# Performance work log

Measured on AMD Instinct MI355X. Metric: run time of the kernel, lower is better.

## Reference

```python
import jax, jax.numpy as jnp
import numpy as np

LAYERS, BLOCKS = 10, 4
RC, DC, SC, EC = 32, 32, 256, 256  # residual, dilation, skip, end channels
CIN, COUT, K = 6, 1, 2
DILATIONS = [2 ** (i % LAYERS) for i in range(BLOCKS * LAYERS)]
NL = len(DILATIONS)


def conv1d(x, w, dilation=1, pad=0):
    # x: [N, C, T], w: [O, I, K]
    return jax.lax.conv_general_dilated(
        x, w, window_strides=(1,), padding=[(pad, pad)],
        rhs_dilation=(dilation,), dimension_numbers=('NCH', 'OIH', 'NCH'))


def setup_inputs() -> dict:
    key = jax.random.key(0)
    ks = jax.random.split(key, 10)
    s = 0.1
    return {
        'x': jax.random.normal(ks[0], (8, CIN, 8192), dtype=jnp.float32),
        'start_w': jax.random.normal(ks[1], (RC, CIN, 1), dtype=jnp.float32) * s,
        'filter_w': jax.random.normal(ks[2], (NL, DC, RC, K), dtype=jnp.float32) * s,
        'gate_w': jax.random.normal(ks[3], (NL, DC, RC, K), dtype=jnp.float32) * s,
        'res_w': jax.random.normal(ks[4], (NL, RC, DC, 1), dtype=jnp.float32) * s,
        'skip_w': jax.random.normal(ks[5], (NL, SC, DC, 1), dtype=jnp.float32) * s,
        'end1_w': jax.random.normal(ks[6], (EC, SC, 1), dtype=jnp.float32) * s,
        'end1_b': jax.random.normal(ks[7], (EC,), dtype=jnp.float32) * s,
        'end2_w': jax.random.normal(ks[8], (COUT, EC, 1), dtype=jnp.float32) * s,
        'end2_b': jax.random.normal(ks[9], (COUT,), dtype=jnp.float32) * s,
    }


def reference(x, start_w, filter_w, gate_w, res_w, skip_w, end1_w, end1_b, end2_w, end2_b):
    x = conv1d(x, start_w)  # [B, RC, T]
    T = x.shape[2]
    # symmetric padding=(K-1)*d makes length grow by d each layer;
    # the shortest skip is the first one: T + (K-1)*DILATIONS[0]
    min_len = T + (K - 1) * DILATIONS[0]
    skip_sum = jnp.zeros((x.shape[0], SC, min_len), dtype=x.dtype)
    for i, d in enumerate(DILATIONS):
        pad = (K - 1) * d
        f = jnp.tanh(conv1d(x, filter_w[i], d, pad))
        g = jax.nn.sigmoid(conv1d(x, gate_w[i], d, pad))
        x = f * g  # [B, DC, T'] with T' = T_prev + d
        s = conv1d(x, skip_w[i])
        skip_sum = skip_sum + s[:, :, -min_len:]
        x = conv1d(x, res_w[i]) + x  # residual add (RC == DC)
    h = jax.nn.relu(skip_sum)
    h = jax.nn.relu(conv1d(h, end1_w) + end1_b[None, :, None])
    h = conv1d(h, end2_w) + end2_b[None, :, None]
    return h[:, :, -1]  # [B, COUT]
```

## Files before the change

kernel.cpp:

```cpp
#include <hip/hip_runtime.h>
#include <hip/hip_fp16.h>
#include <math.h>


#define NL 40
#define TLEN 8192

#define F_BLOB 0
#define F_C0   61440
#define F_Z    61696
#define F_H    71936
#define F_OB   73984
#define F_CNT  73992

__device__ __forceinline__ float wsrc(const float* __restrict__ fw,
                                      const float* __restrict__ gw,
                                      const float* __restrict__ rw,
                                      int l, int ch, int h, int r) {
    const int base = (l * 32 + ch) * 32 + h * 16;
    if (r < 16) return fw[(base + r) * 2];
    if (r < 32) return gw[(base + (r - 16)) * 2];
    return rw[base + (r - 32)];
}

__global__ __launch_bounds__(256) void k1_prep(
    const float* __restrict__ x, const float* __restrict__ start_w,
    const float* __restrict__ filter_w, const float* __restrict__ gate_w,
    const float* __restrict__ res_w, float* __restrict__ ws)
{
    const int blk = blockIdx.x, t = threadIdx.x;
    if (blk < 240) {
        const int p = blk * 256 + t;
        const int l = p / 1536;
        const int rem = p - l * 1536;
        const int i = rem >> 8;
        const int rem2 = rem & 255;
        const int lane = rem2 >> 2;
        const int jp = rem2 & 3;
        const int ch = lane & 31, h = lane >> 5;
        const int r0 = i * 8 + jp * 2;
        const float v0 = wsrc(filter_w, gate_w, res_w, l, ch, h, r0);
        const float v1 = wsrc(filter_w, gate_w, res_w, l, ch, h, r0 + 1);
        ((__half2*)ws)[p] = __floats2half2_rn(v0, v1);
    } else {
        const int b = t >> 5, ch = t & 31;
        float acc = 0.f;
#pragma unroll
        for (int j = 0; j < 6; ++j)
            acc += start_w[ch * 6 + j] * x[(b * 6 + j) * TLEN + TLEN - 1];
        ws[F_C0 + t] = acc;
#pragma unroll
        for (int k = t; k < 2048; k += 256) ws[F_H + k] = 0.f;
        if (t < 8) { ws[F_OB + t] = 0.f; ((int*)(ws + F_CNT))[t] = 0; }
    }
}

struct WBlob { float4 q[6]; };

__device__ __forceinline__ float dot16h(const float4& a, const float4& b,
                                        const float* c) {
    const __half2* h0 = (const __half2*)&a;
    const __half2* h1 = (const __half2*)&b;
    float acc = 0.f;
#pragma unroll
    for (int i = 0; i < 4; ++i) {
        float2 w = __half22float2(h0[i]);
        acc += w.x * c[2*i] + w.y * c[2*i+1];
    }
#pragma unroll
    for (int i = 0; i < 4; ++i) {
        float2 w = __half22float2(h1[i]);
        acc += w.x * c[8+2*i] + w.y * c[8+2*i+1];
    }
    return acc;
}

__device__ __forceinline__ float tanh_fast(float f) {
    f = fminf(fmaxf(f, -15.f), 15.f);
    float e2 = __expf(2.f * f);
    return (e2 - 1.f) / (e2 + 1.f);
}

#define K2_PREFETCH(L4, D) do {                                              \
    if ((L4) < NL) {                                                         \
        _Pragma("unroll")                                                    \
        for (int i = 0; i < 6; ++i)                                          \
            w##D.q[i] = blob[(L4) * 384 + i * 64 + lane];                    \
    }                                                                        \
} while (0)

#define K2_STEP(L, D) do {                                                   \
    float cc[16];                                                            \
    { const float4* cp = (const float4*)(cs + h * 16);                       \
      _Pragma("unroll")                                                      \
      for (int i = 0; i < 4; ++i) ((float4*)cc)[i] = cp[i]; }                \
    float f = dot16h(w##D.q[0], w##D.q[1], cc);                              \
    float g = dot16h(w##D.q[2], w##D.q[3], cc);                              \
    f += __shfl_xor(f, 32, 64);                                              \
    g += __shfl_xor(g, 32, 64);                                              \
    float z = tanh_fast(f) * (1.f / (1.f + __expf(-g)));                     \
    if (h == 0) { zs[ch] = z; zbuf[((L) * 8 + b) * 32 + ch] = z; }           \
    __builtin_amdgcn_wave_barrier();                                         \
    float zz[16];                                                            \
    { const float4* zp = (const float4*)(zs + h * 16);                       \
      _Pragma("unroll")                                                      \
      for (int i = 0; i < 4; ++i) ((float4*)zz)[i] = zp[i]; }                \
    float r = dot16h(w##D.q[4], w##D.q[5], zz);                              \
    r += __shfl_xor(r, 32, 64);                                              \
    float cnew = r + z;                                                      \
    __builtin_amdgcn_wave_barrier();                                         \
    if (h == 0) cs[ch] = cnew;                                               \
    __builtin_amdgcn_wave_barrier();                                         \
    K2_PREFETCH((L) + 4, D);                                                 \
} while (0)

__global__ __launch_bounds__(512) void k2_recur(float* __restrict__ ws)
{
    const int t = threadIdx.x;
    const int b = t >> 6;
    const int lane = t & 63;
    const int ch = lane & 31, h = lane >> 5;

    __shared__ float csm[8][32];
    __shared__ float zsm[8][32];
    float* cs = csm[b];
    float* zs = zsm[b];
    float* zbuf = ws + F_Z;

    if (h == 0) cs[ch] = ws[F_C0 + b * 32 + ch];
    __builtin_amdgcn_wave_barrier();

    const float4* blob = (const float4*)ws;
    WBlob w0, w1, w2, w3;
    K2_PREFETCH(0, 0);
    K2_PREFETCH(1, 1);
    K2_PREFETCH(2, 2);
    K2_PREFETCH(3, 3);

    for (int l = 0; l < NL; l += 4) {
        K2_STEP(l + 0, 0);
        K2_STEP(l + 1, 1);
        K2_STEP(l + 2, 2);
        K2_STEP(l + 3, 3);
    }
}

__global__ __launch_bounds__(256) void k3a_skip(
    const float* __restrict__ skip_w, float* __restrict__ ws)
{
    const int l = blockIdx.x, b = blockIdx.y, t = threadIdx.x;
    __shared__ __align__(16) float zsm[32];
    if (t < 32) zsm[t] = ws[F_Z + (l * 8 + b) * 32 + t];
    __syncthreads();
    const float4* w4 = (const float4*)(skip_w + (size_t)(l * 256 + t) * 32);
    const float4* z4 = (const float4*)zsm;
    float acc = 0.f;
#pragma unroll
    for (int i = 0; i < 8; ++i) {
        float4 wv = w4[i], zv = z4[i];
        acc += wv.x*zv.x + wv.y*zv.y + wv.z*zv.z + wv.w*zv.w;
    }
    atomicAdd(&ws[F_H + b * 256 + t], acc);
}

__global__ __launch_bounds__(256) void k3b_end(
    const float* __restrict__ end1_w, const float* __restrict__ end1_b,
    const float* __restrict__ end2_w, const float* __restrict__ end2_b,
    float* __restrict__ ws, float* __restrict__ out)
{
    const int q = blockIdx.x, b = blockIdx.y, t = threadIdx.x;
    __shared__ __align__(16) float hsm[256];
    __shared__ float psum[64][5];
    const int p = t >> 6, oc = t & 63, row = q * 64 + oc;

    float4 wreg[16];
    const float4* wp = (const float4*)(end1_w + (size_t)row * 256 + p * 64);
#pragma unroll
    for (int i = 0; i < 16; ++i) wreg[i] = wp[i];

    hsm[t] = fmaxf(ws[F_H + b * 256 + t], 0.f);
    __syncthreads();
    const float4* h4 = (const float4*)(hsm + p * 64);
    float acc = 0.f;
#pragma unroll
    for (int i = 0; i < 16; ++i) {
        float4 wv = wreg[i], hv = h4[i];
        acc += wv.x*hv.x + wv.y*hv.y + wv.z*hv.z + wv.w*hv.w;
    }
    psum[oc][p] = acc;
    __syncthreads();
    if (t < 64) {
        const int rr = q * 64 + t;
        float e = psum[t][0] + psum[t][1] + psum[t][2] + psum[t][3]
                + end1_b[rr];
        e = fmaxf(e, 0.f);
        float pe = e * end2_w[rr];
#pragma unroll
        for (int off = 32; off > 0; off >>= 1)
            pe += __shfl_down(pe, off, 64);
        if (t == 0) {
            float* obuf = ws + F_OB;
            int* cnt = (int*)(ws + F_CNT);
            atomicAdd(&obuf[b], pe);
            __threadfence();
            int old = __hip_atomic_fetch_add(&cnt[b], 1, __ATOMIC_ACQ_REL,
                                             __HIP_MEMORY_SCOPE_AGENT);
            if (old == 3) {
                float tot = __hip_atomic_load(&obuf[b], __ATOMIC_ACQUIRE,
                                              __HIP_MEMORY_SCOPE_AGENT);
                out[b] = tot + end2_b[0];
            }
        }
    }
}

extern "C" void kernel_launch(void* const* d_in, const int* in_sizes, int n_in,
                              void* d_out, int out_size, void* d_ws, size_t ws_size,
                              hipStream_t stream) {
    const float* x        = (const float*)d_in[0];
    const float* start_w  = (const float*)d_in[1];
    const float* filter_w = (const float*)d_in[2];
    const float* gate_w   = (const float*)d_in[3];
    const float* res_w    = (const float*)d_in[4];
    const float* skip_w   = (const float*)d_in[5];
    const float* end1_w   = (const float*)d_in[6];
    const float* end1_b   = (const float*)d_in[7];
    const float* end2_w   = (const float*)d_in[8];
    const float* end2_b   = (const float*)d_in[9];
    float* out = (float*)d_out;
    float* ws  = (float*)d_ws;

    k1_prep <<<241, 256, 0, stream>>>(x, start_w, filter_w, gate_w, res_w, ws);
    k2_recur<<<1, 512, 0, stream>>>(ws);
    k3a_skip<<<dim3(NL, 8), 256, 0, stream>>>(skip_w, ws);
    k3b_end <<<dim3(4, 8), 256, 0, stream>>>(end1_w, end1_b, end2_w, end2_b,
                                             ws, out);
}
```

Before: 107.5 us.

## Merge four kernels into two using spin-wait magic flags between blocks

New measurement: 117.6 us. +9.4%, slower.

```diff
diff --git a/kernel.cpp b/kernel.cpp
--- a/kernel.cpp
+++ b/kernel.cpp
@@ -5,13 +5,27 @@
 
 #define NL 40
 #define TLEN 8192
+#define MAGIC 0x13572468
+#define POLL_SLEEP 4
 
 #define F_BLOB 0
-#define F_C0   61440
-#define F_Z    61696
-#define F_H    71936
-#define F_OB   73984
-#define F_CNT  73992
+#define F_Z    61440
+#define F_H    71680
+#define F_OB   73728
+#define F_FLAG 73736
+
+__device__ __forceinline__ void wait_magic(const int* p) {
+    while (__hip_atomic_load(p, __ATOMIC_RELAXED, __HIP_MEMORY_SCOPE_AGENT)
+           != MAGIC)
+        __builtin_amdgcn_s_sleep(POLL_SLEEP);
+    (void)__hip_atomic_load(p, __ATOMIC_ACQUIRE, __HIP_MEMORY_SCOPE_AGENT);
+}
+__device__ __forceinline__ void set_magic(int* p) {
+    __hip_atomic_store(p, MAGIC, __ATOMIC_RELEASE, __HIP_MEMORY_SCOPE_AGENT);
+}
+__device__ __forceinline__ float ldf(const float* p) {
+    return __hip_atomic_load(p, __ATOMIC_RELAXED, __HIP_MEMORY_SCOPE_AGENT);
+}
 
 __device__ __forceinline__ float wsrc(const float* __restrict__ fw,
                                       const float* __restrict__ gw,
@@ -21,38 +35,6 @@
     if (r < 16) return fw[(base + r) * 2];
     if (r < 32) return gw[(base + (r - 16)) * 2];
     return rw[base + (r - 32)];
-}
-
-__global__ __launch_bounds__(256) void k1_prep(
-    const float* __restrict__ x, const float* __restrict__ start_w,
-    const float* __restrict__ filter_w, const float* __restrict__ gate_w,
-    const float* __restrict__ res_w, float* __restrict__ ws)
-{
-    const int blk = blockIdx.x, t = threadIdx.x;
-    if (blk < 240) {
-        const int p = blk * 256 + t;
-        const int l = p / 1536;
-        const int rem = p - l * 1536;
-        const int i = rem >> 8;
-        const int rem2 = rem & 255;
-        const int lane = rem2 >> 2;
-        const int jp = rem2 & 3;
-        const int ch = lane & 31, h = lane >> 5;
-        const int r0 = i * 8 + jp * 2;
-        const float v0 = wsrc(filter_w, gate_w, res_w, l, ch, h, r0);
-        const float v1 = wsrc(filter_w, gate_w, res_w, l, ch, h, r0 + 1);
-        ((__half2*)ws)[p] = __floats2half2_rn(v0, v1);
-    } else {
-        const int b = t >> 5, ch = t & 31;
-        float acc = 0.f;
-#pragma unroll
-        for (int j = 0; j < 6; ++j)
-            acc += start_w[ch * 6 + j] * x[(b * 6 + j) * TLEN + TLEN - 1];
-        ws[F_C0 + t] = acc;
-#pragma unroll
-        for (int k = t; k < 2048; k += 256) ws[F_H + k] = 0.f;
-        if (t < 8) { ws[F_OB + t] = 0.f; ((int*)(ws + F_CNT))[t] = 0; }
-    }
 }
 
 struct WBlob { float4 q[6]; };
@@ -114,9 +96,32 @@
     K2_PREFETCH((L) + 4, D);                                                 \
 } while (0)
 
-__global__ __launch_bounds__(512) void k2_recur(float* __restrict__ ws)
+__global__ __launch_bounds__(512) void ka_repack_recur(
+    const float* __restrict__ x, const float* __restrict__ start_w,
+    const float* __restrict__ filter_w, const float* __restrict__ gate_w,
+    const float* __restrict__ res_w, float* __restrict__ ws)
 {
-    const int t = threadIdx.x;
+    const int blk = blockIdx.x, t = threadIdx.x;
+    int* wf = (int*)(ws + F_FLAG);
+
+    if (blk < 120) {
+        const int p = blk * 512 + t;
+        const int l = p / 1536;
+        const int rem = p - l * 1536;
+        const int i = rem >> 8;
+        const int rem2 = rem & 255;
+        const int lane = rem2 >> 2;
+        const int jp = rem2 & 3;
+        const int ch = lane & 31, h = lane >> 5;
+        const int r0 = i * 8 + jp * 2;
+        const float v0 = wsrc(filter_w, gate_w, res_w, l, ch, h, r0);
+        const float v1 = wsrc(filter_w, gate_w, res_w, l, ch, h, r0 + 1);
+        ((__half2*)ws)[p] = __floats2half2_rn(v0, v1);
+        __syncthreads();
+        if (t == 0) set_magic(&wf[blk]);
+        return;
+    }
+
     const int b = t >> 6;
     const int lane = t & 63;
     const int ch = lane & 31, h = lane >> 5;
@@ -127,8 +132,19 @@
     float* zs = zsm[b];
     float* zbuf = ws + F_Z;
 
-    if (h == 0) cs[ch] = ws[F_C0 + b * 32 + ch];
-    __builtin_amdgcn_wave_barrier();
+    for (int k = t; k < 2048; k += 512) ws[F_H + k] = 0.f;
+    if (t < 8) ws[F_OB + t] = 0.f;
+
+    if (h == 0) {
+        float acc = 0.f;
+#pragma unroll
+        for (int j = 0; j < 6; ++j)
+            acc += start_w[ch * 6 + j] * x[(b * 6 + j) * TLEN + TLEN - 1];
+        cs[ch] = acc;
+    }
+
+    if (t < 120) wait_magic(&wf[t]);
+    __syncthreads();
 
     const float4* blob = (const float4*)ws;
     WBlob w0, w1, w2, w3;
@@ -136,7 +152,6 @@
     K2_PREFETCH(1, 1);
     K2_PREFETCH(2, 2);
     K2_PREFETCH(3, 3);
-
     for (int l = 0; l < NL; l += 4) {
         K2_STEP(l + 0, 0);
         K2_STEP(l + 1, 1);
@@ -145,41 +160,52 @@
     }
 }
 
-__global__ __launch_bounds__(256) void k3a_skip(
-    const float* __restrict__ skip_w, float* __restrict__ ws)
-{
-    const int l = blockIdx.x, b = blockIdx.y, t = threadIdx.x;
-    __shared__ __align__(16) float zsm[32];
-    if (t < 32) zsm[t] = ws[F_Z + (l * 8 + b) * 32 + t];
-    __syncthreads();
-    const float4* w4 = (const float4*)(skip_w + (size_t)(l * 256 + t) * 32);
-    const float4* z4 = (const float4*)zsm;
-    float acc = 0.f;
-#pragma unroll
-    for (int i = 0; i < 8; ++i) {
-        float4 wv = w4[i], zv = z4[i];
-        acc += wv.x*zv.x + wv.y*zv.y + wv.z*zv.z + wv.w*zv.w;
-    }
-    atomicAdd(&ws[F_H + b * 256 + t], acc);
-}
-
-__global__ __launch_bounds__(256) void k3b_end(
+__global__ __launch_bounds__(256) void kb_skip_end(
+    const float* __restrict__ skip_w,
     const float* __restrict__ end1_w, const float* __restrict__ end1_b,
     const float* __restrict__ end2_w, const float* __restrict__ end2_b,
     float* __restrict__ ws, float* __restrict__ out)
 {
-    const int q = blockIdx.x, b = blockIdx.y, t = threadIdx.x;
+    const int id = blockIdx.x, t = threadIdx.x;
+    int* sflag = (int*)(ws + F_FLAG) + 120;
+    int* eflag = sflag + 320;
+    float* hsum = ws + F_H;
+    float* obuf = ws + F_OB;
+
+    if (id < 320) {
+        const int l = id >> 3, b = id & 7;
+        __shared__ __align__(16) float zsm[32];
+        if (t < 32) zsm[t] = ws[F_Z + (l * 8 + b) * 32 + t];
+        __syncthreads();
+        const float4* w4 = (const float4*)(skip_w + (size_t)(l * 256 + t) * 32);
+        const float4* z4 = (const float4*)zsm;
+        float acc = 0.f;
+#pragma unroll
+        for (int i = 0; i < 8; ++i) {
+            float4 wv = w4[i], zv = z4[i];
+            acc += wv.x*zv.x + wv.y*zv.y + wv.z*zv.z + wv.w*zv.w;
+        }
+        atomicAdd(&hsum[b * 256 + t], acc);
+        __syncthreads();
+        if (t == 0) set_magic(&sflag[id]);
+        return;
+    }
+
+    const int e = id - 320, b = e >> 2, q = e & 3;
+    const int p = t >> 6, oc = t & 63, row = q * 64 + oc;
     __shared__ __align__(16) float hsm[256];
     __shared__ float psum[64][5];
-    const int p = t >> 6, oc = t & 63, row = q * 64 + oc;
 
     float4 wreg[16];
     const float4* wp = (const float4*)(end1_w + (size_t)row * 256 + p * 64);
 #pragma unroll
     for (int i = 0; i < 16; ++i) wreg[i] = wp[i];
 
-    hsm[t] = fmaxf(ws[F_H + b * 256 + t], 0.f);
-    __syncthreads();
+    if (t < NL) wait_magic(&sflag[t * 8 + b]);
+    __syncthreads();
+    hsm[t] = fmaxf(ldf(&hsum[b * 256 + t]), 0.f);
+    __syncthreads();
+
     const float4* h4 = (const float4*)(hsm + p * 64);
     float acc = 0.f;
 #pragma unroll
@@ -191,24 +217,22 @@
     __syncthreads();
     if (t < 64) {
         const int rr = q * 64 + t;
-        float e = psum[t][0] + psum[t][1] + psum[t][2] + psum[t][3]
-                + end1_b[rr];
-        e = fmaxf(e, 0.f);
-        float pe = e * end2_w[rr];
+        float ev = psum[t][0] + psum[t][1] + psum[t][2] + psum[t][3]
+                 + end1_b[rr];
+        ev = fmaxf(ev, 0.f);
+        float pe = ev * end2_w[rr];
 #pragma unroll
         for (int off = 32; off > 0; off >>= 1)
             pe += __shfl_down(pe, off, 64);
         if (t == 0) {
-            float* obuf = ws + F_OB;
-            int* cnt = (int*)(ws + F_CNT);
             atomicAdd(&obuf[b], pe);
-            __threadfence();
-            int old = __hip_atomic_fetch_add(&cnt[b], 1, __ATOMIC_ACQ_REL,
-                                             __HIP_MEMORY_SCOPE_AGENT);
-            if (old == 3) {
-                float tot = __hip_atomic_load(&obuf[b], __ATOMIC_ACQUIRE,
-                                              __HIP_MEMORY_SCOPE_AGENT);
-                out[b] = tot + end2_b[0];
+            set_magic(&eflag[b * 4 + q]);
+            if (q == 0) {
+                wait_magic(&eflag[b * 4 + 0]);
+                wait_magic(&eflag[b * 4 + 1]);
+                wait_magic(&eflag[b * 4 + 2]);
+                wait_magic(&eflag[b * 4 + 3]);
+                out[b] = ldf(&obuf[b]) + end2_b[0];
             }
         }
     }
@@ -230,9 +254,8 @@
     float* out = (float*)d_out;
     float* ws  = (float*)d_ws;
 
-    k1_prep <<<241, 256, 0, stream>>>(x, start_w, filter_w, gate_w, res_w, ws);
-    k2_recur<<<1, 512, 0, stream>>>(ws);
-    k3a_skip<<<dim3(NL, 8), 256, 0, stream>>>(skip_w, ws);
-    k3b_end <<<dim3(4, 8), 256, 0, stream>>>(end1_w, end1_b, end2_w, end2_b,
-                                             ws, out);
-}
+    ka_repack_recur<<<121, 512, 0, stream>>>(x, start_w, filter_w, gate_w,
+                                             res_w, ws);
+    kb_skip_end<<<352, 256, 0, stream>>>(skip_w, end1_w, end1_b,
+                                         end2_w, end2_b, ws, out);
+}
```

## Fold residual projection into next layer's filter/gate weights and use fdot2

Applied to the files above, without the earlier changes.

Result: faster. 98.52 us (-8.3%).

```diff
diff --git a/kernel.cpp b/kernel.cpp
--- a/kernel.cpp
+++ b/kernel.cpp
@@ -7,72 +7,26 @@
 #define TLEN 8192
 
 #define F_BLOB 0
-#define F_C0   61440
-#define F_Z    61696
-#define F_H    71936
-#define F_OB   73984
-#define F_CNT  73992
-
-__device__ __forceinline__ float wsrc(const float* __restrict__ fw,
-                                      const float* __restrict__ gw,
-                                      const float* __restrict__ rw,
-                                      int l, int ch, int h, int r) {
-    const int base = (l * 32 + ch) * 32 + h * 16;
-    if (r < 16) return fw[(base + r) * 2];
-    if (r < 32) return gw[(base + (r - 16)) * 2];
-    return rw[base + (r - 32)];
-}
-
-__global__ __launch_bounds__(256) void k1_prep(
-    const float* __restrict__ x, const float* __restrict__ start_w,
-    const float* __restrict__ filter_w, const float* __restrict__ gate_w,
-    const float* __restrict__ res_w, float* __restrict__ ws)
-{
-    const int blk = blockIdx.x, t = threadIdx.x;
-    if (blk < 240) {
-        const int p = blk * 256 + t;
-        const int l = p / 1536;
-        const int rem = p - l * 1536;
-        const int i = rem >> 8;
-        const int rem2 = rem & 255;
-        const int lane = rem2 >> 2;
-        const int jp = rem2 & 3;
-        const int ch = lane & 31, h = lane >> 5;
-        const int r0 = i * 8 + jp * 2;
-        const float v0 = wsrc(filter_w, gate_w, res_w, l, ch, h, r0);
-        const float v1 = wsrc(filter_w, gate_w, res_w, l, ch, h, r0 + 1);
-        ((__half2*)ws)[p] = __floats2half2_rn(v0, v1);
-    } else {
-        const int b = t >> 5, ch = t & 31;
-        float acc = 0.f;
-#pragma unroll
-        for (int j = 0; j < 6; ++j)
-            acc += start_w[ch * 6 + j] * x[(b * 6 + j) * TLEN + TLEN - 1];
-        ws[F_C0 + t] = acc;
-#pragma unroll
-        for (int k = t; k < 2048; k += 256) ws[F_H + k] = 0.f;
-        if (t < 8) { ws[F_OB + t] = 0.f; ((int*)(ws + F_CNT))[t] = 0; }
-    }
-}
-
-struct WBlob { float4 q[6]; };
-
-__device__ __forceinline__ float dot16h(const float4& a, const float4& b,
-                                        const float* c) {
-    const __half2* h0 = (const __half2*)&a;
-    const __half2* h1 = (const __half2*)&b;
-    float acc = 0.f;
-#pragma unroll
-    for (int i = 0; i < 4; ++i) {
-        float2 w = __half22float2(h0[i]);
-        acc += w.x * c[2*i] + w.y * c[2*i+1];
-    }
-#pragma unroll
-    for (int i = 0; i < 4; ++i) {
-        float2 w = __half22float2(h1[i]);
-        acc += w.x * c[8+2*i] + w.y * c[8+2*i+1];
-    }
-    return acc;
+#define F_C0   40960
+#define F_Z    41216
+#define F_H    51456
+#define F_OB   53504
+#define F_CNT  53512
+
+typedef __attribute__((ext_vector_type(2))) _Float16 h2;
+
+#if defined(__has_builtin)
+#if __has_builtin(__builtin_amdgcn_fdot2)
+#define HAS_FDOT2 1
+#endif
+#endif
+
+__device__ __forceinline__ float FDOT2(h2 a, h2 b, float c) {
+#ifdef HAS_FDOT2
+    return __builtin_amdgcn_fdot2(a, b, c, false);
+#else
+    return c + (float)a.x * (float)b.x + (float)a.y * (float)b.y;
+#endif
 }
 
 __device__ __forceinline__ float tanh_fast(float f) {
@@ -81,67 +35,112 @@
     return (e2 - 1.f) / (e2 + 1.f);
 }
 
-#define K2_PREFETCH(L4, D) do {                                              \
-    if ((L4) < NL) {                                                         \
+__global__ __launch_bounds__(256) void k1_fold(
+    const float* __restrict__ x, const float* __restrict__ start_w,
+    const float* __restrict__ filter_w, const float* __restrict__ gate_w,
+    const float* __restrict__ res_w, float* __restrict__ ws)
+{
+    const int l = blockIdx.x, m = blockIdx.y;
+    const int t = threadIdx.x;
+
+    if (l == NL) {
+        if (m == 0) {
+            const int b = t >> 5, ch = t & 31;
+            float acc = 0.f;
+#pragma unroll
+            for (int j = 0; j < 6; ++j)
+                acc += start_w[ch * 6 + j] * x[(b * 6 + j) * TLEN + TLEN - 1];
+            ws[F_C0 + t] = acc;
+            if (t < 8) { ws[F_OB + t] = 0.f; ((int*)(ws + F_CNT))[t] = 0; }
+        } else {
+            for (int k = t; k < 2048; k += 256) ws[F_H + k] = 0.f;
+        }
+        return;
+    }
+
+    __shared__ float F[32][32];
+    __shared__ __align__(16) float R[32][36];
+    const float* src = m ? gate_w : filter_w;
+    for (int e = t; e < 1024; e += 256)
+        F[e >> 5][e & 31] = src[(l * 1024 + e) * 2];
+    if (l > 0)
+        for (int e = t; e < 1024; e += 256) {
+            const int k = e >> 5, j = e & 31;
+            R[k][j] = res_w[(l - 1) * 1024 + e] + (k == j ? 1.f : 0.f);
+        }
+    __syncthreads();
+
+    const int ch = t >> 3, jg = t & 7, j0 = jg * 4;
+    float o0, o1, o2, o3;
+    if (l == 0) {
+        o0 = F[ch][j0]; o1 = F[ch][j0+1]; o2 = F[ch][j0+2]; o3 = F[ch][j0+3];
+    } else {
+        o0 = o1 = o2 = o3 = 0.f;
+#pragma unroll
+        for (int k = 0; k < 32; ++k) {
+            const float fv = F[ch][k];
+            const float4 rv = *(const float4*)&R[k][j0];
+            o0 += fv * rv.x; o1 += fv * rv.y; o2 += fv * rv.z; o3 += fv * rv.w;
+        }
+    }
+    const int hh = jg >> 2;
+    __half* dst = (__half*)ws + (size_t)l * 2048 + (hh * 32 + ch) * 32
+                + (m ? 16 : 0) + (j0 & 15);
+    ((__half2*)dst)[0] = __floats2half2_rn(o0, o1);
+    ((__half2*)dst)[1] = __floats2half2_rn(o2, o3);
+}
+
+#define K2_PREF(L, W) do {                                                   \
+    if ((L) < NL) {                                                          \
         _Pragma("unroll")                                                    \
-        for (int i = 0; i < 6; ++i)                                          \
-            w##D.q[i] = blob[(L4) * 384 + i * 64 + lane];                    \
+        for (int i = 0; i < 4; ++i)                                          \
+            W[i] = blob[(L) * 256 + lane * 4 + i];                           \
     }                                                                        \
 } while (0)
 
-#define K2_STEP(L, D) do {                                                   \
-    float cc[16];                                                            \
-    { const float4* cp = (const float4*)(cs + h * 16);                       \
-      _Pragma("unroll")                                                      \
-      for (int i = 0; i < 4; ++i) ((float4*)cc)[i] = cp[i]; }                \
-    float f = dot16h(w##D.q[0], w##D.q[1], cc);                              \
-    float g = dot16h(w##D.q[2], w##D.q[3], cc);                              \
+#define K2_STEP(L, W) do {                                                   \
+    h2 s[8];                                                                 \
+    { const float4* sp = (const float4*)zsm;                                 \
+      *(float4*)&s[0] = sp[h * 2];                                           \
+      *(float4*)&s[4] = sp[h * 2 + 1]; }                                     \
+    float f = 0.f, g = 0.f;                                                  \
+    const h2* wf = (const h2*)&W[0];                                         \
+    const h2* wg = (const h2*)&W[2];                                         \
+    _Pragma("unroll")                                                        \
+    for (int i = 0; i < 8; ++i) {                                            \
+        f = FDOT2(wf[i], s[i], f);                                           \
+        g = FDOT2(wg[i], s[i], g);                                           \
+    }                                                                        \
     f += __shfl_xor(f, 32, 64);                                              \
     g += __shfl_xor(g, 32, 64);                                              \
     float z = tanh_fast(f) * (1.f / (1.f + __expf(-g)));                     \
-    if (h == 0) { zs[ch] = z; zbuf[((L) * 8 + b) * 32 + ch] = z; }           \
+    if (h == 0) {                                                            \
+        zbuf[((L) * 8 + b) * 32 + ch] = z;                                   \
+        zsm[ch] = __float2half(z);                                           \
+    }                                                                        \
     __builtin_amdgcn_wave_barrier();                                         \
-    float zz[16];                                                            \
-    { const float4* zp = (const float4*)(zs + h * 16);                       \
-      _Pragma("unroll")                                                      \
-      for (int i = 0; i < 4; ++i) ((float4*)zz)[i] = zp[i]; }                \
-    float r = dot16h(w##D.q[4], w##D.q[5], zz);                              \
-    r += __shfl_xor(r, 32, 64);                                              \
-    float cnew = r + z;                                                      \
-    __builtin_amdgcn_wave_barrier();                                         \
-    if (h == 0) cs[ch] = cnew;                                               \
-    __builtin_amdgcn_wave_barrier();                                         \
-    K2_PREFETCH((L) + 4, D);                                                 \
+    K2_PREF((L) + 4, W);                                                     \
 } while (0)
 
-__global__ __launch_bounds__(512) void k2_recur(float* __restrict__ ws)
-{
-    const int t = threadIdx.x;
-    const int b = t >> 6;
-    const int lane = t & 63;
+__global__ __launch_bounds__(64) void k2_recur(float* __restrict__ ws)
+{
+    const int b = blockIdx.x;
+    const int lane = threadIdx.x;
     const int ch = lane & 31, h = lane >> 5;
-
-    __shared__ float csm[8][32];
-    __shared__ float zsm[8][32];
-    float* cs = csm[b];
-    float* zs = zsm[b];
+    __shared__ __align__(16) __half zsm[32];
     float* zbuf = ws + F_Z;
 
-    if (h == 0) cs[ch] = ws[F_C0 + b * 32 + ch];
+    if (h == 0) zsm[ch] = __float2half(ws[F_C0 + b * 32 + ch]);
     __builtin_amdgcn_wave_barrier();
 
     const float4* blob = (const float4*)ws;
-    WBlob w0, w1, w2, w3;
-    K2_PREFETCH(0, 0);
-    K2_PREFETCH(1, 1);
-    K2_PREFETCH(2, 2);
-    K2_PREFETCH(3, 3);
-
+    float4 w0[4], w1[4], w2[4], w3[4];
+    K2_PREF(0, w0); K2_PREF(1, w1); K2_PREF(2, w2); K2_PREF(3, w3);
     for (int l = 0; l < NL; l += 4) {
-        K2_STEP(l + 0, 0);
-        K2_STEP(l + 1, 1);
-        K2_STEP(l + 2, 2);
-        K2_STEP(l + 3, 3);
+        K2_STEP(l + 0, w0);
+        K2_STEP(l + 1, w1);
+        K2_STEP(l + 2, w2);
+        K2_STEP(l + 3, w3);
     }
 }
 
@@ -230,8 +229,9 @@
     float* out = (float*)d_out;
     float* ws  = (float*)d_ws;
 
-    k1_prep <<<241, 256, 0, stream>>>(x, start_w, filter_w, gate_w, res_w, ws);
-    k2_recur<<<1, 512, 0, stream>>>(ws);
+    k1_fold <<<dim3(NL + 1, 2), 256, 0, stream>>>(x, start_w, filter_w,
+                                                  gate_w, res_w, ws);
+    k2_recur<<<8, 64, 0, stream>>>(ws);
     k3a_skip<<<dim3(NL, 8), 256, 0, stream>>>(skip_w, ws);
     k3b_end <<<dim3(4, 8), 256, 0, stream>>>(end1_w, end1_b, end2_w, end2_b,
                                              ws, out);
```
